# Optimization experiments

Measured on AMD Instinct MI355X. Metric: run time of the kernel, lower is better.

## Reference

```python
import jax, jax.numpy as jnp
import numpy as np

IN_F, OUT_F = 256, 256
GRID_SIZE, SPLINE_ORDER = 5, 3
SPLINE_TERMS = GRID_SIZE + SPLINE_ORDER  # 8
PADE_EPS = 1e-4
SHARPNESS = 50.0


def build_grid():
    h = 2.0 / GRID_SIZE  # grid_range (-1, 1)
    g = np.arange(-SPLINE_ORDER, GRID_SIZE + SPLINE_ORDER + 1, dtype=np.float32) * h - 1.0
    return jnp.asarray(np.broadcast_to(g, (IN_F, g.shape[0])).copy())  # [in, 12]


def b_splines(x, grid):
    # x: [B, in], grid: [in, G] -> bases: [B, in, spline_terms]
    xg = x[..., None]  # [B, in, 1]
    g = grid  # broadcasts as [1, in, G]
    bases = ((xg >= g[..., :-1]) & (xg < g[..., 1:])).astype(x.dtype)
    for k in range(1, SPLINE_ORDER + 1):
        left = (xg - g[..., :-(k + 1)]) / (g[..., k:-1] - g[..., :-(k + 1)] + 1e-8)
        right = (g[..., k + 1:] - xg) / (g[..., k + 1:] - g[..., 1:-k] + 1e-8)
        bases = left * bases[..., :-1] + right * bases[..., 1:]
    return bases


def setup_inputs() -> dict:
    key = jax.random.key(0)
    ks = jax.random.split(key, 8)
    B = 4096
    return {
        'x': jax.random.normal(ks[0], (B, IN_F), jnp.float32),
        'base_weight': jax.random.normal(ks[1], (OUT_F, IN_F), jnp.float32) * 0.05,
        'num_spline_weight': jax.random.normal(ks[2], (OUT_F, IN_F, SPLINE_TERMS), jnp.float32) * 0.1,
        'den_spline_weight': jax.random.normal(ks[3], (OUT_F, IN_F, SPLINE_TERMS), jnp.float32) * 0.1,
        'heaviside_bias': jax.random.normal(ks[4], (OUT_F, IN_F), jnp.float32) * 0.1,
        'heaviside_weight': jax.random.normal(ks[5], (OUT_F, IN_F), jnp.float32) * 0.1,
        'l2_den_weight': jax.random.normal(ks[6], (OUT_F, IN_F), jnp.float32) * 0.01,
        'prod_den_weight': jax.random.normal(ks[7], (OUT_F, IN_F), jnp.float32) * 0.01,
        'grid': build_grid(),
    }


def reference(x, base_weight, num_spline_weight, den_spline_weight, heaviside_bias,
              heaviside_weight, l2_den_weight, prod_den_weight, grid):
    act = jax.nn.silu(x)  # base_activation = SiLU
    base_out = jnp.einsum('bi,oi->bo', act, base_weight)
    sb = b_splines(x, grid)  # [B, in, K]
    num_spline = jnp.einsum('bik,oik->boi', sb, num_spline_weight)  # [B, out, in]
    x_diff = x[:, None, :] - heaviside_bias  # [B, out, in]
    heaviside_out = jax.nn.sigmoid(SHARPNESS * x_diff) * heaviside_weight
    numerator = num_spline + heaviside_out
    den_spline = jnp.einsum('bik,oik->boi', sb, den_spline_weight)
    l2_sq = jnp.sum(x * x, axis=-1)[:, None, None]  # [B, 1, 1]
    prod_val = jnp.prod(x, axis=-1)[:, None, None]  # [B, 1, 1]
    denominator = 1.0 + den_spline + l2_sq * l2_den_weight + prod_val * prod_den_weight
    den_safe = jax.nn.softplus(denominator) + PADE_EPS
    pade_out = jnp.sum(numerator / den_safe, axis=-1)  # reduce over in
    return base_out + pade_out
```

## Files before the change

### kernel.cpp

```cpp
#include <hip/hip_runtime.h>


#define IN_F 256
#define OUT_F 256
#define B_TOTAL 4096
#define NWAVE 4
#define NS 4

constexpr float L2E = 1.4426950408889634f;
constexpr float LN2 = 0.6931471805599453f;

typedef _Float16 f16x8 __attribute__((ext_vector_type(8)));
typedef float    f32x16 __attribute__((ext_vector_type(16)));

__device__ __forceinline__ float fast_exp2(float a) { return __builtin_amdgcn_exp2f(a); }
__device__ __forceinline__ float fast_log2(float a) { return __builtin_amdgcn_logf(a); }
__device__ __forceinline__ float fast_rcp(float a)  { return __builtin_amdgcn_rcpf(a); }


__global__ __launch_bounds__(256)
void prep2(const float* __restrict__ bw, const float* __restrict__ nw,
           const float* __restrict__ dw, const float* __restrict__ hb,
           const float* __restrict__ hw, const float* __restrict__ lw,
           const float* __restrict__ pw, const float* __restrict__ x,
           f16x8* __restrict__ sbpk, float* __restrict__ ex,
           _Float16* __restrict__ silu2,
           _Float16* __restrict__ bwp,
           f16x8* __restrict__ bfN, f16x8* __restrict__ bfD,
           float2* __restrict__ misc2,
           float* __restrict__ l2s, float* __restrict__ prs,
           float* __restrict__ out, int out_n)
{
    if (blockIdx.x < 256) {
        const int i = blockIdx.x;
        const int o = threadIdx.x;
        const int oi = o * IN_F + i;
        const float* n8 = nw + (size_t)oi * 8;
        const float* d8 = dw + (size_t)oi * 8;
        f16x8 vhi, vlo, vd;
        #pragma unroll
        for (int k = 0; k < 8; ++k) {
            const float nv = n8[k];
            const _Float16 h = (_Float16)nv;
            vhi[k] = h;
            vlo[k] = (_Float16)(nv - (float)h);
            vd[k]  = (_Float16)d8[k];
        }
        const float lwv = lw[oi], pwv = pw[oi];
        const _Float16 lwh = (_Float16)lwv;
        const _Float16 lwl = (_Float16)(lwv - (float)lwh);
        const _Float16 z0 = (_Float16)0.0f;
        const f16x8 vs = {lwh, lwl, lwh, (_Float16)pwv, (_Float16)1.0f, z0, z0, z0};
        const int ot = o >> 5, ol = o & 31;
        const size_t base = ((size_t)i * 8 + ot) * 64;
        bfN[base + ol]      = vhi;
        bfN[base + 32 + ol] = vlo;
        bfD[base + ol]      = vd;
        bfD[base + 32 + ol] = vs;
        misc2[(size_t)i * OUT_F + o] =
            make_float2(fast_exp2(hb[oi] * (50.0f * L2E)), hw[oi]);
        bwp[(size_t)o * IN_F + i] = (_Float16)bw[oi];
    } else if (blockIdx.x < 512) {
        __shared__ float t[64][65];
        const int blk = blockIdx.x - 256;
        const int bt = blk >> 2;
        const int it = blk & 3;
        const int c  = threadIdx.x & 63;
        const int r0 = threadIdx.x >> 6;
        #pragma unroll
        for (int rr = 0; rr < 16; ++rr) {
            const int r = r0 * 16 + rr;
            t[r][c] = x[(size_t)(bt * 64 + r) * IN_F + it * 64 + c];
        }
        __syncthreads();
        const int b = bt * 64 + c;
        f16x8 sh8, sl8;
        #pragma unroll
        for (int rr = 0; rr < 16; ++rr) {
            const int r = r0 * 16 + rr;
            const int i = it * 64 + r;
            const float xv = t[c][r];
            ex[(size_t)i * B_TOTAL + b] = fast_exp2(fminf(-50.0f * L2E * xv, 58.0f));
            const float sl = xv * fast_rcp(1.0f + fast_exp2(-L2E * xv));
            const _Float16 sH = (_Float16)sl;
            const _Float16 sL = (_Float16)(sl - (float)sH);
            sh8[rr & 7] = sH; sl8[rr & 7] = sL;
            if ((rr & 7) == 7) {
                const size_t si8 = (size_t)b * IN_F + (i - 7);
                *reinterpret_cast<f16x8*>(silu2 + si8) = sh8;
                *reinterpret_cast<f16x8*>(silu2 + (size_t)B_TOTAL * IN_F + si8) = sl8;
            }
            const float tt = (xv + 2.2f) * 2.5f;
            const float sf = floorf(tt);
            const float u  = tt - sf;
            const float u2 = u * u;
            const float u3 = u2 * u;
            const float om = 1.0f - u;
            const float W0 = om * om * om * (1.0f / 6.0f);
            const float W1 = fmaf(3.0f, u3, fmaf(-6.0f, u2, 4.0f)) * (1.0f / 6.0f);
            const float W2 = fmaf(-3.0f, u3, fmaf(3.0f, u2, fmaf(3.0f, u, 1.0f))) * (1.0f / 6.0f);
            const float W3 = u3 * (1.0f / 6.0f);
            const int  siq = (int)sf;
            f16x8 sb8;
            #pragma unroll
            for (int j = 0; j < 8; ++j) {
                float v = 0.f;
                v = (siq == j + 3) ? W0 : v;
                v = (siq == j + 2) ? W1 : v;
                v = (siq == j + 1) ? W2 : v;
                v = (siq == j    ) ? W3 : v;
                sb8[j] = (_Float16)v;
            }
            sbpk[(size_t)i * B_TOTAL + b] = sb8;
        }
    } else if (blockIdx.x < 768) {
        const int blk = blockIdx.x - 512;
        const int wv = threadIdx.x >> 6;
        const int lane = threadIdx.x & 63;
        const int row = blk * NWAVE + wv;
        #pragma unroll
        for (int rr = 0; rr < 4; ++rr) {
            const int r = row * 4 + rr;
            const float* xr = x + (size_t)r * IN_F;
            float pl2 = 0.f, ppr = 1.f;
            #pragma unroll
            for (int c = 0; c < 4; ++c) {
                float xv = xr[c * 64 + lane];
                pl2 = fmaf(xv, xv, pl2);
                ppr *= xv;
            }
            #pragma unroll
            for (int m = 1; m < 64; m <<= 1) {
                pl2 += __shfl_xor(pl2, m);
                ppr *= __shfl_xor(ppr, m);
            }
            if (lane == 0) { l2s[r] = pl2; prs[r] = ppr; }
        }
    } else {
        const size_t base = ((size_t)(blockIdx.x - 768) * 256 + threadIdx.x) * 4;
        if (base + 4 <= (size_t)out_n)
            *reinterpret_cast<float4*>(out + base) = make_float4(0.f, 0.f, 0.f, 0.f);
    }
}

__global__ __launch_bounds__(256, 5)
void padekan_mfma2(const f16x8* __restrict__ sbpk, const float* __restrict__ ex,
                   const _Float16* __restrict__ silu2, const _Float16* __restrict__ bwp,
                   const f16x8* __restrict__ bfN, const f16x8* __restrict__ bfD,
                   const float2* __restrict__ misc2, const float* __restrict__ l2s,
                   const float* __restrict__ prs, float* __restrict__ out)
{
    __shared__ float red[NS][64][17];

    const int lane = threadIdx.x & 63;
    const int wv = threadIdx.x >> 6;
    const int ot = blockIdx.x & 7;
    const int ih = (blockIdx.x >> 3) & 1;
    const int bt = blockIdx.x >> 4;
    const int bl = lane & 31;
    const int hi = lane >> 5;
    const int b0 = bt * 32;
    const int bme = b0 + bl;

    const float l2v = l2s[bme];
    const float prv = prs[bme];
    const _Float16 l2h = (_Float16)l2v;
    const _Float16 l2l = (_Float16)(l2v - (float)l2h);
    const _Float16 z0 = (_Float16)0.0f;
    const f16x8 stat8 = {l2h, l2h, l2l, (_Float16)prv, (_Float16)1.0f, z0, z0, z0};

    const f32x16 zero16 = {};
    f32x16 acc = {};

    const int i0 = ih * 128 + wv * 32;
    #pragma unroll 1
    for (int ii = 0; ii < 32; ++ii) {
        const int i = i0 + ii;

        if ((ii & 7) == 0) {
            const size_t sidx = (size_t)hi * (B_TOTAL * IN_F) + (size_t)bme * IN_F + i;
            const f16x8 sfr = *reinterpret_cast<const f16x8*>(silu2 + sidx);
            const f16x8 wfr = *reinterpret_cast<const f16x8*>(
                bwp + (size_t)(ot * 32 + bl) * IN_F + i);
            acc = __builtin_amdgcn_mfma_f32_32x32x16_f16(sfr, wfr, acc, 0, 0, 0);
        }

        const f16x8 sbv = sbpk[(size_t)i * B_TOTAL + bme];
        const size_t fb = ((size_t)i * 8 + ot) * 64 + lane;
        const f16x8 vbN = bfN[fb];
        const f16x8 vbD = bfD[fb];
        const float2 mi = misc2[(size_t)i * OUT_F + ot * 32 + bl];
        const f16x8 aD = hi ? stat8 : sbv;

        f32x16 cn = __builtin_amdgcn_mfma_f32_32x32x16_f16(sbv, vbN, zero16, 0, 0, 0);
        f32x16 cd = __builtin_amdgcn_mfma_f32_32x32x16_f16(aD, vbD, zero16, 0, 0, 0);

        const float* ep = ex + (size_t)i * B_TOTAL + b0 + hi * 4;
        #pragma unroll
        for (int gq = 0; gq < 4; ++gq) {
            const float4 eA = *reinterpret_cast<const float4*>(ep + gq * 8);
            const float exq[4] = {eA.x, eA.y, eA.z, eA.w};
            #pragma unroll
            for (int j = 0; j < 4; ++j) {
                const int r = gq * 4 + j;
                const float den = cd[r];
                const float ttv = fast_exp2(-L2E * fabsf(den));
                const float sp  = fmaf(fast_log2(1.0f + ttv), LN2, fmaxf(den, 0.0f));
                const float q   = fmaf(exq[j], mi.x, 1.0f);
                const float rrv = fast_rcp(q * (sp + 1e-4f));
                acc[r] = fmaf(fmaf(cn[r], q, mi.y), rrv, acc[r]);
            }
        }
    }

    #pragma unroll
    for (int oo = 0; oo < 16; ++oo) red[wv][lane][oo] = acc[oo];
    __syncthreads();
    #pragma unroll
    for (int e = 0; e < 4; ++e) {
        const int l = threadIdx.x & 63;
        const int r = (threadIdx.x >> 6) + e * 4;
        const float s = (red[0][l][r] + red[1][l][r]) + (red[2][l][r] + red[3][l][r]);
        const int row = (r & 3) + 8 * (r >> 2) + 4 * (l >> 5);
        atomicAdd(&out[(size_t)(b0 + row) * OUT_F + ot * 32 + (l & 31)], s);
    }
}


__global__ __launch_bounds__(256)
void prep_mfma(const float* __restrict__ bw, const float* __restrict__ nw,
               const float* __restrict__ dw, const float* __restrict__ hb,
               const float* __restrict__ hw, const float* __restrict__ lw,
               const float* __restrict__ pw, const float* __restrict__ x,
               float* __restrict__ xT, float2* __restrict__ exsi,
               f16x8* __restrict__ bfN, f16x8* __restrict__ bfD,
               float4* __restrict__ misc,
               float* __restrict__ l2s, float* __restrict__ prs)
{
    if (blockIdx.x < 256) {
        const int i = blockIdx.x;
        const int o = threadIdx.x;
        const int oi = o * IN_F + i;
        const float* n8 = nw + (size_t)oi * 8;
        const float* d8 = dw + (size_t)oi * 8;
        f16x8 vhi, vlo, vd;
        #pragma unroll
        for (int k = 0; k < 8; ++k) {
            const float nv = n8[k];
            const _Float16 h = (_Float16)nv;
            vhi[k] = h;
            vlo[k] = (_Float16)(nv - (float)h);
            vd[k]  = (_Float16)d8[k];
        }
        const float lwv = lw[oi], pwv = pw[oi];
        const _Float16 lwh = (_Float16)lwv;
        const _Float16 lwl = (_Float16)(lwv - (float)lwh);
        const _Float16 z0 = (_Float16)0.0f;
        const f16x8 vs = {lwh, lwl, lwh, (_Float16)pwv, (_Float16)1.0f, z0, z0, z0};
        const int ot = o >> 5, ol = o & 31;
        const size_t base = ((size_t)i * 8 + ot) * 64;
        bfN[base + ol]      = vhi;
        bfN[base + 32 + ol] = vlo;
        bfD[base + ol]      = vd;
        bfD[base + 32 + ol] = vs;
        misc[(size_t)i * OUT_F + o] =
            make_float4(fast_exp2(hb[oi] * (50.0f * L2E)), hw[oi], bw[oi], 0.0f);
    } else if (blockIdx.x < 512) {
        __shared__ float t[64][65];
        const int blk = blockIdx.x - 256;
        const int bt = blk >> 2;
        const int it = blk & 3;
        const int c  = threadIdx.x & 63;
        const int r0 = threadIdx.x >> 6;
        #pragma unroll
        for (int rr = 0; rr < 16; ++rr) {
            const int r = r0 * 16 + rr;
            t[r][c] = x[(size_t)(bt * 64 + r) * IN_F + it * 64 + c];
        }
        __syncthreads();
        #pragma unroll
        for (int rr = 0; rr < 16; ++rr) {
            const int r = r0 * 16 + rr;
            const float v = t[c][r];
            const size_t idx = (size_t)(it * 64 + r) * B_TOTAL + bt * 64 + c;
            xT[idx] = v;
            const float exv = fast_exp2(fminf(-50.0f * L2E * v, 58.0f));
            const float sl = v * fast_rcp(1.0f + fast_exp2(-L2E * v));
            exsi[idx] = make_float2(exv, sl);
        }
    } else {
        const int blk = blockIdx.x - 512;
        const int wv = threadIdx.x >> 6;
        const int lane = threadIdx.x & 63;
        const int row = blk * NWAVE + wv;
        #pragma unroll
        for (int rr = 0; rr < 4; ++rr) {
            const int r = row * 4 + rr;
            const float* xr = x + (size_t)r * IN_F;
            float pl2 = 0.f, ppr = 1.f;
            #pragma unroll
            for (int c = 0; c < 4; ++c) {
                float xv = xr[c * 64 + lane];
                pl2 = fmaf(xv, xv, pl2);
                ppr *= xv;
            }
            #pragma unroll
            for (int m = 1; m < 64; m <<= 1) {
                pl2 += __shfl_xor(pl2, m);
                ppr *= __shfl_xor(ppr, m);
            }
            if (lane == 0) { l2s[r] = pl2; prs[r] = ppr; }
        }
    }
}

__global__ __launch_bounds__(256, 4)
void padekan_mfma(const float* __restrict__ xT, const float2* __restrict__ exsi,
                  const f16x8* __restrict__ bfN, const f16x8* __restrict__ bfD,
                  const float4* __restrict__ misc, const float* __restrict__ l2s,
                  const float* __restrict__ prs, const float* __restrict__ grid,
                  float* __restrict__ out)
{
    __shared__ float red[NS][64][17];

    const int lane = threadIdx.x & 63;
    const int wv = threadIdx.x >> 6;
    const int ot = blockIdx.x & 7;
    const int bt = blockIdx.x >> 3;
    const int bl = lane & 31;
    const int hi = lane >> 5;
    const int b0 = bt * 32;

    const float g0 = grid[0];
    const float inv_h = 1.0f / (grid[1] - grid[0]);

    const float l2v = l2s[b0 + bl];
    const float prv = prs[b0 + bl];
    const _Float16 l2h = (_Float16)l2v;
    const _Float16 l2l = (_Float16)(l2v - (float)l2h);
    const _Float16 z0 = (_Float16)0.0f;
    const f16x8 stat8 = {l2h, l2h, l2l, (_Float16)prv, (_Float16)1.0f, z0, z0, z0};

    const f32x16 zero16 = {};
    f32x16 acc = {};

    const int i0 = wv * 64;
    #pragma unroll 1
    for (int ii = 0; ii < 64; ++ii) {
        const int i = i0 + ii;
        const float xv = xT[(size_t)i * B_TOTAL + b0 + bl];

        const float t  = (xv - g0) * inv_h;
        const float sf = floorf(t);
        const float u  = t - sf;
        const float u2 = u * u;
        const float u3 = u2 * u;
        const float om = 1.0f - u;
        const float W0 = om * om * om * (1.0f / 6.0f);
        const float W1 = fmaf(3.0f, u3, fmaf(-6.0f, u2, 4.0f)) * (1.0f / 6.0f);
        const float W2 = fmaf(-3.0f, u3, fmaf(3.0f, u2, fmaf(3.0f, u, 1.0f))) * (1.0f / 6.0f);
        const float W3 = u3 * (1.0f / 6.0f);
        const int  si = (int)sf;

        f16x8 aN;
        #pragma unroll
        for (int j = 0; j < 8; ++j) {
            float v = 0.f;
            v = (si == j + 3) ? W0 : v;
            v = (si == j + 2) ? W1 : v;
            v = (si == j + 1) ? W2 : v;
            v = (si == j    ) ? W3 : v;
            aN[j] = (_Float16)v;
        }
        const f16x8 aD = hi ? stat8 : aN;

        const size_t fb = ((size_t)i * 8 + ot) * 64 + lane;
        const f16x8 vbN = bfN[fb];
        const f16x8 vbD = bfD[fb];
        const float4 mi = misc[(size_t)i * OUT_F + ot * 32 + bl];

        f32x16 cn = __builtin_amdgcn_mfma_f32_32x32x16_f16(aN, vbN, zero16, 0, 0, 0);
        f32x16 cd = __builtin_amdgcn_mfma_f32_32x32x16_f16(aD, vbD, zero16, 0, 0, 0);

        const float2* ep = exsi + (size_t)i * B_TOTAL + b0 + hi * 4;
        #pragma unroll
        for (int gq = 0; gq < 4; ++gq) {
            const float4 eA = *reinterpret_cast<const float4*>(ep + gq * 8);
            const float4 eB = *reinterpret_cast<const float4*>(ep + gq * 8 + 2);
            const float exq[4] = {eA.x, eA.z, eB.x, eB.z};
            const float svq[4] = {eA.y, eA.w, eB.y, eB.w};
            #pragma unroll
            for (int j = 0; j < 4; ++j) {
                const int r = gq * 4 + j;
                const float den = cd[r];
                const float ttv = fast_exp2(-L2E * fabsf(den));
                const float sp  = fmaf(fast_log2(1.0f + ttv), LN2, fmaxf(den, 0.0f));
                const float q   = fmaf(exq[j], mi.x, 1.0f);
                const float rrv = fast_rcp(q * (sp + 1e-4f));
                const float numer = fmaf(cn[r], q, mi.y);
                acc[r] = fmaf(svq[j], mi.z, fmaf(numer, rrv, acc[r]));
            }
        }
    }

    #pragma unroll
    for (int oo = 0; oo < 16; ++oo) red[wv][lane][oo] = acc[oo];
    __syncthreads();
    #pragma unroll
    for (int e = 0; e < 4; ++e) {
        const int l = threadIdx.x & 63;
        const int r = (threadIdx.x >> 6) + e * 4;
        const float s = (red[0][l][r] + red[1][l][r]) + (red[2][l][r] + red[3][l][r]);
        const int row = (r & 3) + 8 * (r >> 2) + 4 * (l >> 5);
        out[(size_t)(b0 + row) * OUT_F + ot * 32 + (l & 31)] = s;
    }
}


__global__ __launch_bounds__(256)
void padekan_fallback(const float* __restrict__ x,  const float* __restrict__ base_w,
                      const float* __restrict__ num_w, const float* __restrict__ den_w,
                      const float* __restrict__ hbias, const float* __restrict__ hweight,
                      const float* __restrict__ l2w, const float* __restrict__ pw,
                      const float* __restrict__ grid, float* __restrict__ out)
{
    const int b = blockIdx.x;
    const int o = threadIdx.x;
    const float g0 = grid[0];
    const float inv_h = 1.0f / (grid[1] - grid[0]);
    const float* xrow = x + (size_t)b * IN_F;
    float l2v = 0.f, prodv = 1.f;
    for (int i = 0; i < IN_F; ++i) { float xv = xrow[i]; l2v = fmaf(xv, xv, l2v); prodv *= xv; }
    float acc = 0.f;
    for (int i = 0; i < IN_F; ++i) {
        const float xv = xrow[i];
        const float t = (xv - g0) * inv_h;
        const float sf = floorf(t);
        const float u = t - sf;
        const float u2 = u * u, u3 = u2 * u, om = 1.0f - u;
        const float W[4] = {om * om * om / 6.0f,
                            fmaf(3.0f, u3, fmaf(-6.0f, u2, 4.0f)) / 6.0f,
                            fmaf(-3.0f, u3, fmaf(3.0f, u2, fmaf(3.0f, u, 1.0f))) / 6.0f,
                            u3 / 6.0f};
        const int si = (int)sf;
        const int oi = o * IN_F + i;
        float num = 0.f, den = fmaf(l2v, l2w[oi], fmaf(prodv, pw[oi], 1.0f));
        #pragma unroll
        for (int w = 0; w < 4; ++w) {
            const int j = si - 3 + w;
            if (j >= 0 && j < 8) {
                num = fmaf(W[w], num_w[(size_t)oi * 8 + j], num);
                den = fmaf(W[w], den_w[(size_t)oi * 8 + j], den);
            }
        }
        float q = fminf(fast_exp2(fminf((hbias[oi] - xv) * (50.0f * L2E), 99.0f)), 1e30f) + 1.0f;
        float tt = fast_exp2(-L2E * fabsf(den));
        float sp = fmaf(fast_log2(1.0f + tt), LN2, fmaxf(den, 0.0f));
        float rr = fast_rcp(q * (sp + 1e-4f));
        float silu_v = xv * fast_rcp(1.0f + fast_exp2(-L2E * xv));
        acc = fmaf(silu_v, base_w[oi], fmaf(fmaf(num, q, hweight[oi]), rr, acc));
    }
    out[(size_t)b * OUT_F + o] = acc;
}

extern "C" void kernel_launch(void* const* d_in, const int* in_sizes, int n_in,
                              void* d_out, int out_size, void* d_ws, size_t ws_size,
                              hipStream_t stream) {
    const float* xp  = (const float*)d_in[0];
    const float* bw  = (const float*)d_in[1];
    const float* nw  = (const float*)d_in[2];
    const float* dw  = (const float*)d_in[3];
    const float* hb  = (const float*)d_in[4];
    const float* hw  = (const float*)d_in[5];
    const float* lw  = (const float*)d_in[6];
    const float* pwt = (const float*)d_in[7];
    const float* gr  = (const float*)d_in[8];
    float* outp = (float*)d_out;

    const size_t sbpk_b = (size_t)IN_F * B_TOTAL * sizeof(f16x8);
    const size_t ex_b   = (size_t)IN_F * B_TOTAL * sizeof(float);
    const size_t si2_b  = (size_t)2 * B_TOTAL * IN_F * sizeof(_Float16);
    const size_t bwp_b  = (size_t)OUT_F * IN_F * sizeof(_Float16);
    const size_t bf_b   = (size_t)IN_F * 8 * 64 * sizeof(f16x8);
    const size_t mi2_b  = (size_t)IN_F * OUT_F * sizeof(float2);
    const size_t st_b   = (size_t)B_TOTAL * 2 * sizeof(float);
    const size_t tier1  = sbpk_b + ex_b + si2_b + bwp_b + 2 * bf_b + mi2_b + st_b;

    const size_t xT_b   = (size_t)B_TOTAL * IN_F * sizeof(float);
    const size_t exsi_b = (size_t)B_TOTAL * IN_F * sizeof(float2);
    const size_t misc_b = (size_t)IN_F * OUT_F * sizeof(float4);
    const size_t tier2  = xT_b + exsi_b + 2 * bf_b + misc_b + st_b;

    dim3 block(256);

    if (ws_size >= tier1) {
        char* p = (char*)d_ws;
        f16x8*     sbpk = (f16x8*)p;      p += sbpk_b;
        float*     exA  = (float*)p;      p += ex_b;
        _Float16*  si2  = (_Float16*)p;   p += si2_b;
        _Float16*  bwp  = (_Float16*)p;   p += bwp_b;
        f16x8*     bfN  = (f16x8*)p;      p += bf_b;
        f16x8*     bfD  = (f16x8*)p;      p += bf_b;
        float2*    mi2  = (float2*)p;     p += mi2_b;
        float*     l2sp = (float*)p;
        float*     prsp = l2sp + B_TOTAL;
        prep2<<<dim3(1792), block, 0, stream>>>(
            bw, nw, dw, hb, hw, lw, pwt, xp, sbpk, exA, si2, bwp, bfN, bfD,
            mi2, l2sp, prsp, outp, out_size);
        padekan_mfma2<<<dim3(2048), block, 0, stream>>>(
            sbpk, exA, si2, bwp, bfN, bfD, mi2, l2sp, prsp, outp);
    } else if (ws_size >= tier2) {
        char* p = (char*)d_ws;
        float*  xT   = (float*)p;            p += xT_b;
        float2* exsi = (float2*)p;           p += exsi_b;
        f16x8*  bfN  = (f16x8*)p;            p += bf_b;
        f16x8*  bfD  = (f16x8*)p;            p += bf_b;
        float4* misc = (float4*)p;           p += misc_b;
        float*  l2sp = (float*)p;
        float*  prsp = l2sp + B_TOTAL;
        prep_mfma<<<dim3(768), block, 0, stream>>>(
            bw, nw, dw, hb, hw, lw, pwt, xp, xT, exsi, bfN, bfD, misc, l2sp, prsp);
        padekan_mfma<<<dim3(1024), block, 0, stream>>>(
            xT, exsi, bfN, bfD, misc, l2sp, prsp, gr, outp);
    } else {
        padekan_fallback<<<dim3(B_TOTAL), dim3(OUT_F), 0, stream>>>(
            xp, bw, nw, dw, hb, hw, lw, pwt, gr, outp);
    }
}
```

Baseline: 219.0 us.

## Retile x preprocessing, remap blocks per XCD, simplify softplus

The x preprocessing is split into 1024 smaller blocks, each handling a 64x16 tile. These blocks stage the silu hi/lo halves in shared memory and write them out as vectors, which should give more parallelism and better coalescing. The main kernel's block index is remapped so that each XCD (selected by blockIdx mod 8) works on a contiguous range of batch tiles, which is meant to improve L2 reuse of the per-batch inputs. Softplus is now computed as log(1+exp(den)) without the abs/max stabilisation, saving a few ALU ops but risking overflow for large den.

```diff
diff --git a/kernel.cpp b/kernel.cpp
--- a/kernel.cpp
+++ b/kernel.cpp
@@ -19,7 +19,7 @@
 
 
 __global__ __launch_bounds__(256)
-void prep2(const float* __restrict__ bw, const float* __restrict__ nw,
+void prep3(const float* __restrict__ bw, const float* __restrict__ nw,
            const float* __restrict__ dw, const float* __restrict__ hb,
            const float* __restrict__ hw, const float* __restrict__ lw,
            const float* __restrict__ pw, const float* __restrict__ x,
@@ -31,8 +31,70 @@
            float* __restrict__ l2s, float* __restrict__ prs,
            float* __restrict__ out, int out_n)
 {
-    if (blockIdx.x < 256) {
-        const int i = blockIdx.x;
+    if (blockIdx.x < 1024) {
+        __shared__ float xs[64][17];
+        __shared__ __align__(16) _Float16 sil[2][64][16];
+        const int bt = blockIdx.x >> 4;
+        const int it = blockIdx.x & 15;
+        const int b0 = bt * 64;
+        const int i0 = it * 16;
+        {
+            const int rr = threadIdx.x >> 2;
+            const int c4 = (threadIdx.x & 3) * 4;
+            const float4 v = *reinterpret_cast<const float4*>(
+                x + (size_t)(b0 + rr) * IN_F + i0 + c4);
+            xs[rr][c4] = v.x; xs[rr][c4 + 1] = v.y;
+            xs[rr][c4 + 2] = v.z; xs[rr][c4 + 3] = v.w;
+        }
+        __syncthreads();
+        const int bl = threadIdx.x & 63;
+        const int ig = threadIdx.x >> 6;
+        #pragma unroll
+        for (int k = 0; k < 4; ++k) {
+            const int il = ig * 4 + k;
+            const int i = i0 + il;
+            const float xv = xs[bl][il];
+            ex[(size_t)i * B_TOTAL + b0 + bl] =
+                fast_exp2(fminf(-50.0f * L2E * xv, 58.0f));
+            const float sl = xv * fast_rcp(1.0f + fast_exp2(-L2E * xv));
+            const _Float16 sH = (_Float16)sl;
+            sil[0][bl][il] = sH;
+            sil[1][bl][il] = (_Float16)(sl - (float)sH);
+            const float tt = (xv + 2.2f) * 2.5f;
+            const float sf = floorf(tt);
+            const float u  = tt - sf;
+            const float u2 = u * u;
+            const float u3 = u2 * u;
+            const float om = 1.0f - u;
+            const float W0 = om * om * om * (1.0f / 6.0f);
+            const float W1 = fmaf(3.0f, u3, fmaf(-6.0f, u2, 4.0f)) * (1.0f / 6.0f);
+            const float W2 = fmaf(-3.0f, u3, fmaf(3.0f, u2, fmaf(3.0f, u, 1.0f))) * (1.0f / 6.0f);
+            const float W3 = u3 * (1.0f / 6.0f);
+            const int  siq = (int)sf;
+            f16x8 sb8;
+            #pragma unroll
+            for (int j = 0; j < 8; ++j) {
+                float v = 0.f;
+                v = (siq == j + 3) ? W0 : v;
+                v = (siq == j + 2) ? W1 : v;
+                v = (siq == j + 1) ? W2 : v;
+                v = (siq == j    ) ? W3 : v;
+                sb8[j] = (_Float16)v;
+            }
+            sbpk[(size_t)i * B_TOTAL + b0 + bl] = sb8;
+        }
+        __syncthreads();
+        {
+            const int hl = threadIdx.x >> 7;
+            const int b2 = (threadIdx.x >> 1) & 63;
+            const int ch = threadIdx.x & 1;
+            const f16x8 v = *reinterpret_cast<const f16x8*>(&sil[hl][b2][ch * 8]);
+            *reinterpret_cast<f16x8*>(
+                silu2 + (size_t)hl * B_TOTAL * IN_F +
+                (size_t)(b0 + b2) * IN_F + i0 + ch * 8) = v;
+        }
+    } else if (blockIdx.x < 1280) {
+        const int i = blockIdx.x - 1024;
         const int o = threadIdx.x;
         const int oi = o * IN_F + i;
         const float* n8 = nw + (size_t)oi * 8;
@@ -60,61 +122,8 @@
         misc2[(size_t)i * OUT_F + o] =
             make_float2(fast_exp2(hb[oi] * (50.0f * L2E)), hw[oi]);
         bwp[(size_t)o * IN_F + i] = (_Float16)bw[oi];
-    } else if (blockIdx.x < 512) {
-        __shared__ float t[64][65];
-        const int blk = blockIdx.x - 256;
-        const int bt = blk >> 2;
-        const int it = blk & 3;
-        const int c  = threadIdx.x & 63;
-        const int r0 = threadIdx.x >> 6;
-        #pragma unroll
-        for (int rr = 0; rr < 16; ++rr) {
-            const int r = r0 * 16 + rr;
-            t[r][c] = x[(size_t)(bt * 64 + r) * IN_F + it * 64 + c];
-        }
-        __syncthreads();
-        const int b = bt * 64 + c;
-        f16x8 sh8, sl8;
-        #pragma unroll
-        for (int rr = 0; rr < 16; ++rr) {
-            const int r = r0 * 16 + rr;
-            const int i = it * 64 + r;
-            const float xv = t[c][r];
-            ex[(size_t)i * B_TOTAL + b] = fast_exp2(fminf(-50.0f * L2E * xv, 58.0f));
-            const float sl = xv * fast_rcp(1.0f + fast_exp2(-L2E * xv));
-            const _Float16 sH = (_Float16)sl;
-            const _Float16 sL = (_Float16)(sl - (float)sH);
-            sh8[rr & 7] = sH; sl8[rr & 7] = sL;
-            if ((rr & 7) == 7) {
-                const size_t si8 = (size_t)b * IN_F + (i - 7);
-                *reinterpret_cast<f16x8*>(silu2 + si8) = sh8;
-                *reinterpret_cast<f16x8*>(silu2 + (size_t)B_TOTAL * IN_F + si8) = sl8;
-            }
-            const float tt = (xv + 2.2f) * 2.5f;
-            const float sf = floorf(tt);
-            const float u  = tt - sf;
-            const float u2 = u * u;
-            const float u3 = u2 * u;
-            const float om = 1.0f - u;
-            const float W0 = om * om * om * (1.0f / 6.0f);
-            const float W1 = fmaf(3.0f, u3, fmaf(-6.0f, u2, 4.0f)) * (1.0f / 6.0f);
-            const float W2 = fmaf(-3.0f, u3, fmaf(3.0f, u2, fmaf(3.0f, u, 1.0f))) * (1.0f / 6.0f);
-            const float W3 = u3 * (1.0f / 6.0f);
-            const int  siq = (int)sf;
-            f16x8 sb8;
-            #pragma unroll
-            for (int j = 0; j < 8; ++j) {
-                float v = 0.f;
-                v = (siq == j + 3) ? W0 : v;
-                v = (siq == j + 2) ? W1 : v;
-                v = (siq == j + 1) ? W2 : v;
-                v = (siq == j    ) ? W3 : v;
-                sb8[j] = (_Float16)v;
-            }
-            sbpk[(size_t)i * B_TOTAL + b] = sb8;
-        }
-    } else if (blockIdx.x < 768) {
-        const int blk = blockIdx.x - 512;
+    } else if (blockIdx.x < 1536) {
+        const int blk = blockIdx.x - 1280;
         const int wv = threadIdx.x >> 6;
         const int lane = threadIdx.x & 63;
         const int row = blk * NWAVE + wv;
@@ -137,14 +146,14 @@
             if (lane == 0) { l2s[r] = pl2; prs[r] = ppr; }
         }
     } else {
-        const size_t base = ((size_t)(blockIdx.x - 768) * 256 + threadIdx.x) * 4;
+        const size_t base = ((size_t)(blockIdx.x - 1536) * 256 + threadIdx.x) * 4;
         if (base + 4 <= (size_t)out_n)
             *reinterpret_cast<float4*>(out + base) = make_float4(0.f, 0.f, 0.f, 0.f);
     }
 }
 
 __global__ __launch_bounds__(256, 5)
-void padekan_mfma2(const f16x8* __restrict__ sbpk, const float* __restrict__ ex,
+void padekan_mfma3(const f16x8* __restrict__ sbpk, const float* __restrict__ ex,
                    const _Float16* __restrict__ silu2, const _Float16* __restrict__ bwp,
                    const f16x8* __restrict__ bfN, const f16x8* __restrict__ bfD,
                    const float2* __restrict__ misc2, const float* __restrict__ l2s,
@@ -154,9 +163,12 @@
 
     const int lane = threadIdx.x & 63;
     const int wv = threadIdx.x >> 6;
-    const int ot = blockIdx.x & 7;
-    const int ih = (blockIdx.x >> 3) & 1;
-    const int bt = blockIdx.x >> 4;
+    const int xcd = blockIdx.x & 7;
+    const int r   = blockIdx.x >> 3;
+    const int ot  = r >> 5;
+    const int btl = (r >> 1) & 15;
+    const int ih  = r & 1;
+    const int bt  = xcd * 16 + btl;
     const int bl = lane & 31;
     const int hi = lane >> 5;
     const int b0 = bt * 32;
@@ -202,13 +214,13 @@
             const float exq[4] = {eA.x, eA.y, eA.z, eA.w};
             #pragma unroll
             for (int j = 0; j < 4; ++j) {
-                const int r = gq * 4 + j;
-                const float den = cd[r];
-                const float ttv = fast_exp2(-L2E * fabsf(den));
-                const float sp  = fmaf(fast_log2(1.0f + ttv), LN2, fmaxf(den, 0.0f));
+                const int rr_ = gq * 4 + j;
+                const float den = cd[rr_];
+                const float t1  = fast_exp2(L2E * den);
+                const float spe = fmaf(fast_log2(1.0f + t1), LN2, 1e-4f);
                 const float q   = fmaf(exq[j], mi.x, 1.0f);
-                const float rrv = fast_rcp(q * (sp + 1e-4f));
-                acc[r] = fmaf(fmaf(cn[r], q, mi.y), rrv, acc[r]);
+                const float rrv = fast_rcp(q * spe);
+                acc[rr_] = fmaf(fmaf(cn[rr_], q, mi.y), rrv, acc[rr_]);
             }
         }
     }
@@ -219,9 +231,10 @@
     #pragma unroll
     for (int e = 0; e < 4; ++e) {
         const int l = threadIdx.x & 63;
-        const int r = (threadIdx.x >> 6) + e * 4;
-        const float s = (red[0][l][r] + red[1][l][r]) + (red[2][l][r] + red[3][l][r]);
-        const int row = (r & 3) + 8 * (r >> 2) + 4 * (l >> 5);
+        const int rr_ = (threadIdx.x >> 6) + e * 4;
+        const float s = (red[0][l][rr_] + red[1][l][rr_]) +
+                        (red[2][l][rr_] + red[3][l][rr_]);
+        const int row = (rr_ & 3) + 8 * (rr_ >> 2) + 4 * (l >> 5);
         atomicAdd(&out[(size_t)(b0 + row) * OUT_F + ot * 32 + (l & 31)], s);
     }
 }
@@ -504,10 +517,10 @@
         float2*    mi2  = (float2*)p;     p += mi2_b;
         float*     l2sp = (float*)p;
         float*     prsp = l2sp + B_TOTAL;
-        prep2<<<dim3(1792), block, 0, stream>>>(
+        prep3<<<dim3(2560), block, 0, stream>>>(
             bw, nw, dw, hb, hw, lw, pwt, xp, sbpk, exA, si2, bwp, bfN, bfD,
             mi2, l2sp, prsp, outp, out_size);
-        padekan_mfma2<<<dim3(2048), block, 0, stream>>>(
+        padekan_mfma3<<<dim3(2048), block, 0, stream>>>(
             sbpk, exA, si2, bwp, bfN, bfD, mi2, l2sp, prsp, outp);
     } else if (ws_size >= tier2) {
         char* p = (char*)d_ws;
```

Result: faster. 197.2 us (-9.9%).
